# Kernel tuning notes

Hardware: AMD Instinct MI355X
Metric: run time of the kernel (lower is better)

## Reference

```python
import jax, jax.numpy as jnp
import numpy as np

N_NODES = 100000
N_EDGES = 3200000
D_IN = 128
D_HID = 128
N_CLASSES = 40


def setup_inputs() -> dict:
    key = jax.random.key(0)
    ks = jax.random.split(key, 8)
    x = jax.random.normal(ks[0], (N_NODES, D_IN), dtype=jnp.float32)
    edge_index = jax.random.randint(ks[1], (2, N_EDGES), 0, N_NODES, dtype=jnp.int64)
    s1 = 1.0 / np.sqrt(D_IN)
    s2 = 1.0 / np.sqrt(D_HID)
    W1 = jax.random.normal(ks[2], (D_IN, D_HID), dtype=jnp.float32) * s1
    b1 = jnp.zeros((D_HID,), dtype=jnp.float32)
    W2 = jax.random.normal(ks[3], (D_HID, D_HID), dtype=jnp.float32) * s2
    b2 = jnp.zeros((D_HID,), dtype=jnp.float32)
    Wl = jax.random.normal(ks[4], (D_HID, N_CLASSES), dtype=jnp.float32) * s2
    bl = jnp.zeros((N_CLASSES,), dtype=jnp.float32)
    return {"x": x, "edge_index": edge_index, "W1": W1, "b1": b1,
            "W2": W2, "b2": b2, "Wl": Wl, "bl": bl}


def _gcn_conv(x, W, b, src, dst, inv_sqrt_deg, n_nodes):
    # h = X @ W  (linear transform first: cheaper when out_dim <= in_dim)
    h = x @ W  # [N, d_out]
    # symmetric normalization: norm_e = deg(src)^-1/2 * deg(dst)^-1/2
    norm = inv_sqrt_deg[src] * inv_sqrt_deg[dst]  # [E]
    msg = h[src] * norm[:, None]                  # gather + scale  [E, d_out]
    out = jax.ops.segment_sum(msg, dst, num_segments=n_nodes)  # scatter-add
    return out + b


def reference(x, edge_index, W1, b1, W2, b2, Wl, bl):
    n = x.shape[0]
    # GCNConv adds self-loops before normalization (PyG default)
    loops = jnp.arange(n, dtype=edge_index.dtype)
    src = jnp.concatenate([edge_index[0], loops])
    dst = jnp.concatenate([edge_index[1], loops])
    deg = jax.ops.segment_sum(jnp.ones_like(dst, dtype=x.dtype), dst, num_segments=n)
    inv_sqrt_deg = jnp.where(deg > 0, jax.lax.rsqrt(deg), 0.0)

    h = _gcn_conv(x, W1, b1, src, dst, inv_sqrt_deg, n)
    h = jax.nn.relu(h)
    h = _gcn_conv(h, W2, b2, src, dst, inv_sqrt_deg, n)
    h = jax.nn.relu(h)
    return h @ Wl + bl
```

## Files before the change

kernel.cpp:

```cpp
#include <hip/hip_runtime.h>
#include <hip/hip_bf16.h>

typedef _Float16 f16;
typedef _Float16 f16x8 __attribute__((ext_vector_type(8)));

#define D 128
#define N_CLS 40
#define BN 128
#define NBMAX 1024


__global__ __launch_bounds__(256) void k_hist(const int* __restrict__ dst,
                                              int* __restrict__ bcnt, int e) {
  __shared__ int lh[NBMAX];
  for (int j = threadIdx.x; j < NBMAX; j += 256) lh[j] = 0;
  __syncthreads();
  int stride = gridDim.x * blockDim.x;
  for (int q = blockIdx.x * blockDim.x + threadIdx.x; q < e; q += stride)
    atomicAdd(&lh[dst[q] >> 7], 1);
  __syncthreads();
  for (int j = threadIdx.x; j < NBMAX; j += 256)
    if (lh[j]) atomicAdd(&bcnt[j], lh[j]);
}

__global__ __launch_bounds__(1024) void k_bscan(const int* __restrict__ bcnt,
                                                int* __restrict__ bbase,
                                                int* __restrict__ bcur) {
  __shared__ int sums[NBMAX];
  int t = threadIdx.x;
  int c = bcnt[t];
  sums[t] = c;
  __syncthreads();
  for (int off = 1; off < NBMAX; off <<= 1) {
    int a = (t >= off) ? sums[t - off] : 0;
    __syncthreads();
    sums[t] += a;
    __syncthreads();
  }
  bbase[t] = sums[t] - c;
  bcur[t] = sums[t] - c;
}

__global__ __launch_bounds__(256) void k_place(const int* __restrict__ src,
                                               const int* __restrict__ dst,
                                               int* __restrict__ bcur,
                                               unsigned int* __restrict__ binned,
                                               int e, int nwg) {
  __shared__ int lh[NBMAX];
  __shared__ int lofs[NBMAX];
  __shared__ int lcur[NBMAX];
  int chunk = (e + nwg - 1) / nwg;
  int lo = blockIdx.x * chunk;
  int hi = min(e, lo + chunk);
  int t = threadIdx.x;
  for (int j = t; j < NBMAX; j += 256) { lh[j] = 0; lcur[j] = 0; }
  __syncthreads();
  for (int q = lo + t; q < hi; q += 256) atomicAdd(&lh[dst[q] >> 7], 1);
  __syncthreads();
  for (int j = t; j < NBMAX; j += 256) {
    int c = lh[j];
    lofs[j] = c ? atomicAdd(&bcur[j], c) : 0;
  }
  __syncthreads();
  for (int q = lo + t; q < hi; q += 256) {
    int d = dst[q];
    int b = d >> 7;
    int r = atomicAdd(&lcur[b], 1);
    binned[lofs[b] + r] = ((unsigned int)(d & 127) << 17) | (unsigned int)src[q];
  }
}

__global__ __launch_bounds__(256) void k_csr(const unsigned int* __restrict__ binned,
                                             const int* __restrict__ bbase,
                                             int* __restrict__ csr,
                                             int* __restrict__ deg,
                                             float* __restrict__ isd,
                                             int* __restrict__ row_start, int n) {
  int b = blockIdx.x;
  int lo = bbase[b], hi = bbase[b + 1];
  __shared__ int h[BN];
  __shared__ int sc[BN];
  __shared__ int cur[BN];
  int t = threadIdx.x;
  if (t < BN) h[t] = 0;
  __syncthreads();
  for (int q = lo + t; q < hi; q += 256) atomicAdd(&h[binned[q] >> 17], 1);
  __syncthreads();
  if (t < BN) sc[t] = h[t];
  __syncthreads();
  for (int off = 1; off < BN; off <<= 1) {
    int a = 0;
    if (t < BN && t >= off) a = sc[t - off];
    __syncthreads();
    if (t < BN) sc[t] += a;
    __syncthreads();
  }
  if (t < BN) {
    int excl = sc[t] - h[t];
    cur[t] = lo + excl;
    int i = b * BN + t;
    if (i < n) {
      deg[i] = h[t];
      isd[i] = rsqrtf((float)(h[t] + 1));
      row_start[i] = lo + excl;
    }
  }
  __syncthreads();
  for (int q = lo + t; q < hi; q += 256) {
    unsigned int u = binned[q];
    int p = atomicAdd(&cur[u >> 17], 1);
    csr[p] = (int)(u & 0x1FFFF);
  }
}

template <bool HALF_IN>
__global__ __launch_bounds__(256) void k_gemm_t(const void* __restrict__ Xv,
                                                const float* __restrict__ W,
                                                const float* __restrict__ isd,
                                                f16* __restrict__ HS, int n) {
  __shared__ float Xt[64][D + 4];
  __shared__ float Wb[32][D + 4];
  const size_t ss = (size_t)n * 16;
  int t = threadIdx.x;
  int r0 = blockIdx.x * 64;
  if (!HALF_IN) {
    const float* X = (const float*)Xv;
    for (int q = t; q < 64 * 32; q += 256) {
      int row = q >> 5, cb = (q & 31) << 2;
      float4 v = {0.f, 0.f, 0.f, 0.f};
      if (r0 + row < n) v = *(const float4*)(X + (size_t)(r0 + row) * D + cb);
      *(float4*)&Xt[row][cb] = v;
    }
  } else {
    const f16* X = (const f16*)Xv;
    for (int q = t; q < 64 * 16; q += 256) {
      int row = q >> 4, cb = (q & 15) << 3;
      f16x8 v = 0;
      if (r0 + row < n) v = *(const f16x8*)(X + (size_t)(r0 + row) * D + cb);
      float* xp = &Xt[row][cb];
#pragma unroll
      for (int j = 0; j < 8; ++j) xp[j] = (float)v[j];
    }
  }
  int tr = ((t >> 4) & 15) << 2;
  int tc = (t & 15) << 3;
  float acc[4][8];
#pragma unroll
  for (int i = 0; i < 4; ++i)
#pragma unroll
    for (int j = 0; j < 8; ++j) acc[i][j] = 0.f;

  for (int hh = 0; hh < 4; ++hh) {
    __syncthreads();
    for (int q = t; q < 32 * 32; q += 256) {
      int row = q >> 5, cb = (q & 31) << 2;
      *(float4*)&Wb[row][cb] = *(const float4*)(W + (size_t)(hh * 32 + row) * D + cb);
    }
    __syncthreads();
#pragma unroll 4
    for (int k = 0; k < 32; ++k) {
      float4 u0 = *(const float4*)&Wb[k][tc];
      float4 u1 = *(const float4*)&Wb[k][tc + 4];
      float bv[8] = {u0.x, u0.y, u0.z, u0.w, u1.x, u1.y, u1.z, u1.w};
      int kk = hh * 32 + k;
#pragma unroll
      for (int i = 0; i < 4; ++i) {
        float a = Xt[tr + i][kk];
#pragma unroll
        for (int j = 0; j < 8; ++j) acc[i][j] += a * bv[j];
      }
    }
  }
#pragma unroll
  for (int i = 0; i < 4; ++i) {
    int row = r0 + tr + i;
    if (row < n) {
      float s = isd[row];
      f16x8 ov;
#pragma unroll
      for (int j = 0; j < 8; ++j) ov[j] = (f16)(s * acc[i][j]);
      *(f16x8*)(HS + (size_t)(tc >> 4) * ss + (size_t)row * 16 + (tc & 15)) = ov;
    }
  }
}

__device__ inline f16x8 shfl_xor_f16x8(f16x8 v, int m) {
  union { f16x8 h; int i[4]; } u;
  u.h = v;
#pragma unroll
  for (int k = 0; k < 4; ++k) u.i[k] = __shfl_xor(u.i[k], m);
  return u.h;
}

__global__ __launch_bounds__(256) void k_aggs(const f16* __restrict__ HS,
                                              const int* __restrict__ csr,
                                              const int* __restrict__ row_start,
                                              const int* __restrict__ deg,
                                              const float* __restrict__ isd,
                                              const float* __restrict__ bias,
                                              f16* __restrict__ G, int n) {
  const size_t ss = (size_t)n * 16;
  int t = threadIdx.x;
  int wave = t >> 6, lane = t & 63;
  int g = lane >> 4, r = lane & 15;
  int s = blockIdx.x & 7;
  int i0 = ((blockIdx.x >> 3) << 4) + (wave << 2) + g;
  bool ok = i0 < n;
  int i = ok ? i0 : n - 1;
  int hf = r & 1, er = r >> 1;
  int dg = deg[i];
  const int* cp = csr + row_start[i];
  const f16* sb = HS + (size_t)s * ss + (size_t)(hf << 3);
  f16x8 a0 = (f16x8)0, a1 = (f16x8)0, a2 = (f16x8)0, a3 = (f16x8)0;
  int iA = cp[er];
  int iB = cp[er + 8];
  int iC = cp[er + 16];
  int iD = cp[er + 24];
  for (int u = 0; u < dg; u += 32) {
    int cA = iA, cB = iB, cC = iC, cD = iD;
    iA = cp[u + 32 + er];
    iB = cp[u + 40 + er];
    iC = cp[u + 48 + er];
    iD = cp[u + 56 + er];
    if (u + er < dg)
      a0 += *(const f16x8*)(sb + ((size_t)(unsigned)cA << 4));
    if (u + 8 + er < dg)
      a1 += *(const f16x8*)(sb + ((size_t)(unsigned)cB << 4));
    if (u + 16 + er < dg)
      a2 += *(const f16x8*)(sb + ((size_t)(unsigned)cC << 4));
    if (u + 24 + er < dg)
      a3 += *(const f16x8*)(sb + ((size_t)(unsigned)cD << 4));
  }
  f16x8 tv = (a0 + a1) + (a2 + a3);
  tv += shfl_xor_f16x8(tv, 2);
  tv += shfl_xor_f16x8(tv, 4);
  tv += shfl_xor_f16x8(tv, 8);
  f16x8 sv = *(const f16x8*)(HS + (size_t)s * ss + (size_t)i * 16 + (hf << 3));
  float di = isd[i];
  const float* bp = bias + s * 16 + (hf << 3);
  float4 b0 = *(const float4*)bp;
  float4 b1 = *(const float4*)(bp + 4);
  float bv[8] = {b0.x, b0.y, b0.z, b0.w, b1.x, b1.y, b1.z, b1.w};
  f16x8 ov;
#pragma unroll
  for (int j = 0; j < 8; ++j) {
    float v = di * ((float)tv[j] + (float)sv[j]) + bv[j];
    v = v > 0.f ? v : 0.f;
    ov[j] = (f16)v;
  }
  if (ok && r < 2)
    *(f16x8*)(G + (size_t)i * D + s * 16 + (hf << 3)) = ov;
}

__global__ __launch_bounds__(256) void k_cls(const f16* __restrict__ H,
                                             const float* __restrict__ Wl,
                                             const float* __restrict__ bl,
                                             float* __restrict__ out, int n) {
  __shared__ float wt[N_CLS][D];
  int t = threadIdx.x;
  for (int q = t; q < D * N_CLS; q += 256) {
    int k = q / N_CLS, c = q - k * N_CLS;
    wt[c][k] = Wl[q];
  }
  int wv = t >> 6, lane = t & 63, g = lane >> 4, l = lane & 15;
  float bb0 = bl[l];
  float bb1 = bl[16 + l];
  float bb2 = (l < 8) ? bl[32 + l] : 0.f;
  __syncthreads();
  int node0 = (blockIdx.x << 7) + (wv << 2) + g;
  for (int it = 0; it < 8; ++it) {
    int node = node0 + it * 16;
    if (node >= n) break;
    f16x8 h = *(const f16x8*)(H + (size_t)node * D + l * 8);
    float hf[8];
#pragma unroll
    for (int j = 0; j < 8; ++j) hf[j] = (float)h[j];
    float r0 = bb0, r1 = bb1, r2 = bb2;
#pragma unroll 4
    for (int c = 0; c < N_CLS; ++c) {
      const float* wp = &wt[c][l * 8];
      float4 w0 = *(const float4*)wp;
      float4 w1 = *(const float4*)(wp + 4);
      float p = hf[0] * w0.x + hf[1] * w0.y + hf[2] * w0.z + hf[3] * w0.w +
                hf[4] * w1.x + hf[5] * w1.y + hf[6] * w1.z + hf[7] * w1.w;
      p += __shfl_xor(p, 1);
      p += __shfl_xor(p, 2);
      p += __shfl_xor(p, 4);
      p += __shfl_xor(p, 8);
      if ((c & 15) == l) {
        if (c < 16) r0 += p;
        else if (c < 32) r1 += p;
        else r2 += p;
      }
    }
    float* op = out + (size_t)node * N_CLS;
    op[l] = r0;
    op[16 + l] = r1;
    if (l < 8) op[32 + l] = r2;
  }
}

extern "C" void kernel_launch(void* const* d_in, const int* in_sizes, int n_in,
                              void* d_out, int out_size, void* d_ws, size_t ws_size,
                              hipStream_t stream) {
  const float* x  = (const float*)d_in[0];
  const int*   ei = (const int*)d_in[1];
  const float* W1 = (const float*)d_in[2];
  const float* b1 = (const float*)d_in[3];
  const float* W2 = (const float*)d_in[4];
  const float* b2 = (const float*)d_in[5];
  const float* Wl = (const float*)d_in[6];
  const float* bl = (const float*)d_in[7];
  float* out = (float*)d_out;

  const int n = in_sizes[0] / D;
  const int e = in_sizes[1] / 2;
  const int* src = ei;
  const int* dst = ei + e;
  const int nb = (n + BN - 1) / BN;

  char* ws = (char*)d_ws;
  size_t off = 0;
  auto alloc = [&](size_t bytes) -> void* {
    void* p = ws + off;
    off += (bytes + 255) & ~(size_t)255;
    return p;
  };
  int*   bcnt      = (int*)alloc(NBMAX * 4);
  int*   bbase     = (int*)alloc(NBMAX * 4);
  int*   bcur      = (int*)alloc(NBMAX * 4);
  int*   deg       = (int*)alloc((size_t)n * 4);
  int*   row_start = (int*)alloc((size_t)n * 4);
  float* isd       = (float*)alloc((size_t)n * 4);
  int*   csr       = (int*)alloc(((size_t)e + 64) * 4);
  f16*   hA        = (f16*)alloc((size_t)n * D * 2);
  f16*   hB        = (f16*)alloc((size_t)n * D * 2);
  unsigned int* binned = (unsigned int*)hA;

  hipMemsetAsync(bcnt, 0, NBMAX * 4, stream);
  hipMemsetAsync(csr + e, 0, 64 * 4, stream);

  const int nwg_place = 512;
  k_hist<<<1024, 256, 0, stream>>>(dst, bcnt, e);
  k_bscan<<<1, 1024, 0, stream>>>(bcnt, bbase, bcur);
  k_place<<<nwg_place, 256, 0, stream>>>(src, dst, bcur, binned, e, nwg_place);
  k_csr<<<nb, 256, 0, stream>>>(binned, bbase, csr, deg, isd, row_start, n);

  int gblocks = (n + 63) / 64;
  int ablocks = ((n + 15) / 16) * 8;
  k_gemm_t<false><<<gblocks, 256, 0, stream>>>(x, W1, isd, hA, n);
  k_aggs<<<ablocks, 256, 0, stream>>>(hA, csr, row_start, deg, isd, b1, hB, n);
  k_gemm_t<true><<<gblocks, 256, 0, stream>>>(hB, W2, isd, hA, n);
  k_aggs<<<ablocks, 256, 0, stream>>>(hA, csr, row_start, deg, isd, b2, hB, n);
  k_cls<<<(n + 127) / 128, 256, 0, stream>>>(hB, Wl, bl, out, n);
}
```

Baseline: 693.9 us.

## Use fp16 MFMA for feature transforms and slim the aggregation gather loop

Replaces the scalar fp32 FMA GEMM with an MFMA 16x16x32 f16 kernel that stages X and a transposed fp16 copy of W in shared memory. It also shrinks the aggregation inner loop from four to two in-flight gathers per lane, using 32-bit byte offsets. The self-loop normalization is recomputed from the degree instead of loading isd. Inputs and weights are now rounded to fp16 before the multiply, which lowers accuracy. Halving the gathers in flight may also hurt latency hiding in the memory-bound aggregation.

```diff
diff --git a/kernel.cpp b/kernel.cpp
--- a/kernel.cpp
+++ b/kernel.cpp
@@ -2,7 +2,9 @@
 #include <hip/hip_bf16.h>
 
 typedef _Float16 f16;
+typedef _Float16 f16x4 __attribute__((ext_vector_type(4)));
 typedef _Float16 f16x8 __attribute__((ext_vector_type(8)));
+typedef float f32x4 __attribute__((ext_vector_type(4)));
 
 #define D 128
 #define N_CLS 40
@@ -114,12 +116,12 @@
 }
 
 template <bool HALF_IN>
-__global__ __launch_bounds__(256) void k_gemm_t(const void* __restrict__ Xv,
+__global__ __launch_bounds__(256) void k_gemm_m(const void* __restrict__ Xv,
                                                 const float* __restrict__ W,
                                                 const float* __restrict__ isd,
                                                 f16* __restrict__ HS, int n) {
-  __shared__ float Xt[64][D + 4];
-  __shared__ float Wb[32][D + 4];
+  __shared__ f16 At[64][136];
+  __shared__ f16 Wt[128][136];
   const size_t ss = (size_t)n * 16;
   int t = threadIdx.x;
   int r0 = blockIdx.x * 64;
@@ -129,7 +131,8 @@
       int row = q >> 5, cb = (q & 31) << 2;
       float4 v = {0.f, 0.f, 0.f, 0.f};
       if (r0 + row < n) v = *(const float4*)(X + (size_t)(r0 + row) * D + cb);
-      *(float4*)&Xt[row][cb] = v;
+      f16x4 h = {(f16)v.x, (f16)v.y, (f16)v.z, (f16)v.w};
+      *(f16x4*)&At[row][cb] = h;
     }
   } else {
     const f16* X = (const f16*)Xv;
@@ -137,49 +140,41 @@
       int row = q >> 4, cb = (q & 15) << 3;
       f16x8 v = 0;
       if (r0 + row < n) v = *(const f16x8*)(X + (size_t)(r0 + row) * D + cb);
-      float* xp = &Xt[row][cb];
-#pragma unroll
-      for (int j = 0; j < 8; ++j) xp[j] = (float)v[j];
-    }
-  }
-  int tr = ((t >> 4) & 15) << 2;
-  int tc = (t & 15) << 3;
-  float acc[4][8];
-#pragma unroll
-  for (int i = 0; i < 4; ++i)
-#pragma unroll
-    for (int j = 0; j < 8; ++j) acc[i][j] = 0.f;
-
-  for (int hh = 0; hh < 4; ++hh) {
-    __syncthreads();
-    for (int q = t; q < 32 * 32; q += 256) {
-      int row = q >> 5, cb = (q & 31) << 2;
-      *(float4*)&Wb[row][cb] = *(const float4*)(W + (size_t)(hh * 32 + row) * D + cb);
-    }
-    __syncthreads();
-#pragma unroll 4
-    for (int k = 0; k < 32; ++k) {
-      float4 u0 = *(const float4*)&Wb[k][tc];
-      float4 u1 = *(const float4*)&Wb[k][tc + 4];
-      float bv[8] = {u0.x, u0.y, u0.z, u0.w, u1.x, u1.y, u1.z, u1.w};
-      int kk = hh * 32 + k;
-#pragma unroll
-      for (int i = 0; i < 4; ++i) {
-        float a = Xt[tr + i][kk];
-#pragma unroll
-        for (int j = 0; j < 8; ++j) acc[i][j] += a * bv[j];
-      }
-    }
-  }
-#pragma unroll
-  for (int i = 0; i < 4; ++i) {
-    int row = r0 + tr + i;
-    if (row < n) {
-      float s = isd[row];
-      f16x8 ov;
-#pragma unroll
-      for (int j = 0; j < 8; ++j) ov[j] = (f16)(s * acc[i][j]);
-      *(f16x8*)(HS + (size_t)(tc >> 4) * ss + (size_t)row * 16 + (tc & 15)) = ov;
+      *(f16x8*)&At[row][cb] = v;
+    }
+  }
+  for (int q = t; q < D * D; q += 256) {
+    int k = q >> 7, c = q & 127;
+    Wt[c][k] = (f16)W[q];
+  }
+  __syncthreads();
+
+  int wave = t >> 6, lane = t & 63;
+  int lw = lane & 15, kg = lane >> 4;
+  f32x4 acc[8];
+#pragma unroll
+  for (int ct = 0; ct < 8; ++ct) acc[ct] = (f32x4)0.f;
+#pragma unroll
+  for (int ks = 0; ks < 4; ++ks) {
+    f16x8 af = *(const f16x8*)&At[(wave << 4) + lw][ks * 32 + kg * 8];
+#pragma unroll
+    for (int ct = 0; ct < 8; ++ct) {
+      f16x8 bf = *(const f16x8*)&Wt[ct * 16 + lw][ks * 32 + kg * 8];
+      acc[ct] = __builtin_amdgcn_mfma_f32_16x16x32_f16(af, bf, acc[ct], 0, 0, 0);
+    }
+  }
+  int rbase = r0 + (wave << 4) + (kg << 2);
+  float sv[4];
+#pragma unroll
+  for (int rr = 0; rr < 4; ++rr)
+    sv[rr] = (rbase + rr < n) ? isd[rbase + rr] : 0.f;
+#pragma unroll
+  for (int ct = 0; ct < 8; ++ct) {
+#pragma unroll
+    for (int rr = 0; rr < 4; ++rr) {
+      int node = rbase + rr;
+      if (node < n)
+        HS[(size_t)ct * ss + (size_t)node * 16 + lw] = (f16)(acc[ct][rr] * sv[rr]);
     }
   }
 }
@@ -196,7 +191,6 @@
                                               const int* __restrict__ csr,
                                               const int* __restrict__ row_start,
                                               const int* __restrict__ deg,
-                                              const float* __restrict__ isd,
                                               const float* __restrict__ bias,
                                               f16* __restrict__ G, int n) {
   const size_t ss = (size_t)n * 16;
@@ -210,33 +204,27 @@
   int hf = r & 1, er = r >> 1;
   int dg = deg[i];
   const int* cp = csr + row_start[i];
-  const f16* sb = HS + (size_t)s * ss + (size_t)(hf << 3);
-  f16x8 a0 = (f16x8)0, a1 = (f16x8)0, a2 = (f16x8)0, a3 = (f16x8)0;
+  const char* sbase = (const char*)(HS + (size_t)s * ss);
+  unsigned hofs = (unsigned)(hf << 4);
+  f16x8 a0 = (f16x8)0, a1 = (f16x8)0;
   int iA = cp[er];
   int iB = cp[er + 8];
-  int iC = cp[er + 16];
-  int iD = cp[er + 24];
-  for (int u = 0; u < dg; u += 32) {
-    int cA = iA, cB = iB, cC = iC, cD = iD;
-    iA = cp[u + 32 + er];
-    iB = cp[u + 40 + er];
-    iC = cp[u + 48 + er];
-    iD = cp[u + 56 + er];
+  for (int u = 0; u < dg; u += 16) {
+    unsigned oA = ((unsigned)iA << 5) + hofs;
+    unsigned oB = ((unsigned)iB << 5) + hofs;
+    iA = cp[u + 16 + er];
+    iB = cp[u + 24 + er];
     if (u + er < dg)
-      a0 += *(const f16x8*)(sb + ((size_t)(unsigned)cA << 4));
+      a0 += *(const f16x8*)(sbase + oA);
     if (u + 8 + er < dg)
-      a1 += *(const f16x8*)(sb + ((size_t)(unsigned)cB << 4));
-    if (u + 16 + er < dg)
-      a2 += *(const f16x8*)(sb + ((size_t)(unsigned)cC << 4));
-    if (u + 24 + er < dg)
-      a3 += *(const f16x8*)(sb + ((size_t)(unsigned)cD << 4));
-  }
-  f16x8 tv = (a0 + a1) + (a2 + a3);
+      a1 += *(const f16x8*)(sbase + oB);
+  }
+  f16x8 tv = a0 + a1;
   tv += shfl_xor_f16x8(tv, 2);
   tv += shfl_xor_f16x8(tv, 4);
   tv += shfl_xor_f16x8(tv, 8);
-  f16x8 sv = *(const f16x8*)(HS + (size_t)s * ss + (size_t)i * 16 + (hf << 3));
-  float di = isd[i];
+  f16x8 svv = *(const f16x8*)(sbase + ((unsigned)i << 5) + hofs);
+  float di = rsqrtf((float)(dg + 1));
   const float* bp = bias + s * 16 + (hf << 3);
   float4 b0 = *(const float4*)bp;
   float4 b1 = *(const float4*)(bp + 4);
@@ -244,7 +232,7 @@
   f16x8 ov;
 #pragma unroll
   for (int j = 0; j < 8; ++j) {
-    float v = di * ((float)tv[j] + (float)sv[j]) + bv[j];
+    float v = di * ((float)tv[j] + (float)svv[j]) + bv[j];
     v = v > 0.f ? v : 0.f;
     ov[j] = (f16)v;
   }
@@ -348,9 +336,9 @@
 
   int gblocks = (n + 63) / 64;
   int ablocks = ((n + 15) / 16) * 8;
-  k_gemm_t<false><<<gblocks, 256, 0, stream>>>(x, W1, isd, hA, n);
-  k_aggs<<<ablocks, 256, 0, stream>>>(hA, csr, row_start, deg, isd, b1, hB, n);
-  k_gemm_t<true><<<gblocks, 256, 0, stream>>>(hB, W2, isd, hA, n);
-  k_aggs<<<ablocks, 256, 0, stream>>>(hA, csr, row_start, deg, isd, b2, hB, n);
+  k_gemm_m<false><<<gblocks, 256, 0, stream>>>(x, W1, isd, hA, n);
+  k_aggs<<<ablocks, 256, 0, stream>>>(hA, csr, row_start, deg, b1, hB, n);
+  k_gemm_m<true><<<gblocks, 256, 0, stream>>>(hB, W2, isd, hA, n);
+  k_aggs<<<ablocks, 256, 0, stream>>>(hA, csr, row_start, deg, b2, hB, n);
   k_cls<<<(n + 127) / 128, 256, 0, stream>>>(hB, Wl, bl, out, n);
 }
```

New measurement: 657.9 us. 1.05x faster.
